# Kernel optimization log

Hardware: AMD Instinct MI355X
Metric: run time of the kernel (lower is better)

Reference implementation:

```python
import jax, jax.numpy as jnp
import numpy as np

N = 10000      # nodes
E = 160000     # edges
B = 4          # batch
D = 256        # in_dim == out_dim
H = 4          # heads
DH = D // H    # per-head dim = 64
L = 2          # num_layers
BACK = 2       # back_look
HID = 128      # hidden_dim
NEG = 0.1      # leaky relu slope


def setup_inputs() -> dict:
    key = jax.random.key(0)
    ks = jax.random.split(key, 12)
    solutions = jax.random.normal(ks[0], (BACK, B, N, HID), dtype=jnp.float32)
    src = jax.random.randint(ks[1], (E,), 0, N)
    dst = jax.random.randint(ks[2], (E,), 0, N)
    w = jax.random.uniform(ks[3], (E,), dtype=jnp.float32)
    fc_w = jax.random.normal(ks[4], (L, D, D), dtype=jnp.float32) * (1.0 / np.sqrt(D))
    attn_l = jax.random.normal(ks[5], (L, H, DH), dtype=jnp.float32) * 0.1
    attn_r = jax.random.normal(ks[6], (L, H, DH), dtype=jnp.float32) * 0.1
    out_fc_w = jax.random.normal(ks[7], (L, DH, DH), dtype=jnp.float32) * (1.0 / np.sqrt(DH))
    out_fc_b = jnp.zeros((L, DH), dtype=jnp.float32)
    mlp_w = jax.random.normal(ks[8], (D, L * D), dtype=jnp.float32) * (1.0 / np.sqrt(L * D))
    mlp_b = jnp.zeros((D,), dtype=jnp.float32)
    return dict(solutions=solutions, w=w, fc_w=fc_w, attn_l=attn_l, attn_r=attn_r,
                out_fc_w=out_fc_w, out_fc_b=out_fc_b, mlp_w=mlp_w, mlp_b=mlp_b,
                src=src, dst=dst)


def _gat_layer(x, w, fc_w, al, ar, ofc_w, ofc_b, src, dst):
    # x: [B,N,D] -> feat: [N,B,H,DH]  (matches torch view+transpose)
    feat = jnp.einsum('bnd,ed->bne', x, fc_w).reshape(B, N, H, DH).transpose(1, 0, 2, 3)
    el = (feat * al).sum(-1)  # [N,B,H]
    er = (feat * ar).sum(-1)  # [N,B,H]
    # edge scores, weighted pre-softmax by edge weight w
    e = jax.nn.leaky_relu(el[src] + er[dst], NEG) * w[:, None, None]  # [E,B,H]
    # edge softmax per destination node (numerically stable)
    m = jax.ops.segment_max(e, dst, num_segments=N)        # [N,B,H]
    ex = jnp.exp(e - m[dst])
    s = jax.ops.segment_sum(ex, dst, num_segments=N)       # [N,B,H]
    a = ex / s[dst]                                        # [E,B,H]
    # weighted scatter-aggregate: u_mul_e + sum
    msg = feat[src] * a[..., None]                         # [E,B,H,DH]
    rst = jax.ops.segment_sum(msg, dst, num_segments=N)    # [N,B,H,DH]
    rst = jax.nn.relu(jnp.einsum('nbhf,of->nbho', rst, ofc_w) + ofc_b)
    # transpose + concat heads -> [B,N,H*DH]
    return rst.transpose(1, 0, 2, 3).reshape(B, N, H * DH)


def reference(solutions, w, fc_w, attn_l, attn_r, out_fc_w, out_fc_b, mlp_w, mlp_b, src, dst):
    # concat back_look solutions along feature dim -> [B,N,D]
    x = jnp.concatenate([solutions[i] for i in range(BACK)], axis=-1)
    outs = []
    for l in range(L):
        x = _gat_layer(x, w, fc_w[l], attn_l[l], attn_r[l],
                       out_fc_w[l], out_fc_b[l], src, dst)
        outs.append(x)
    h = jnp.concatenate(outs, axis=-1)           # [B,N,L*D]
    return h @ mlp_w.T + mlp_b                   # [B,N,D]
```

## Files before the change

kernel.cpp:

```cpp
#include <hip/hip_runtime.h>
#include <math.h>

#define NN 10000
#define NE 160000
#define NB 4
#define NH 4
#define ND 256
#define NT (NN * 16)
#define NM 40000

typedef _Float16 f16;
typedef _Float16 half8 __attribute__((ext_vector_type(8)));
typedef _Float16 h2 __attribute__((ext_vector_type(2)));
typedef float f32x4 __attribute__((ext_vector_type(4)));

union H4 { uint2 u; f16 h[4]; };
union U2H { unsigned u; h2 h; };
union U4H { uint4 u; h2 h[4]; };

__device__ __forceinline__ void gload_lds16(const void* g, void* l) {
  __builtin_amdgcn_global_load_lds((const __attribute__((address_space(1))) void*)g,
                                   (__attribute__((address_space(3))) void*)l, 16, 0, 0);
}

__global__ __launch_bounds__(256) void k_deg(const int* __restrict__ dst, int* __restrict__ deg) {
  int e = blockIdx.x * 256 + threadIdx.x;
  if (e < NE) atomicAdd(&deg[dst[e]], 1);
}

__global__ __launch_bounds__(1024) void k_scan2(const int* __restrict__ deg, int* __restrict__ offs) {
  __shared__ int wsum[16];
  __shared__ int wbase[17];
  const int t = threadIdx.x, lane = t & 63, wv = t >> 6;
  int v[10];
  int s = 0;
  if (t < 1000) {
#pragma unroll
    for (int i = 0; i < 10; ++i) { v[i] = deg[t * 10 + i]; s += v[i]; }
  }
  int inc = s;
#pragma unroll
  for (int k = 1; k < 64; k <<= 1) {
    int u = __shfl_up(inc, k);
    if (lane >= k) inc += u;
  }
  if (lane == 63) wsum[wv] = inc;
  __syncthreads();
  if (t == 0) {
    int c = 0;
#pragma unroll
    for (int i = 0; i < 16; ++i) { wbase[i] = c; c += wsum[i]; }
    wbase[16] = c;
    offs[NN] = c;
  }
  __syncthreads();
  if (t < 1000) {
    int c = wbase[wv] + inc - s;
#pragma unroll
    for (int i = 0; i < 10; ++i) { offs[t * 10 + i] = c; c += v[i]; }
  }
}

__global__ __launch_bounds__(256) void k_scatter(const int* __restrict__ src, const int* __restrict__ dst,
                                                 const float* __restrict__ w, const int* __restrict__ offs,
                                                 int* __restrict__ cursor, int* __restrict__ csr_src,
                                                 float* __restrict__ csr_w) {
  int e = blockIdx.x * 256 + threadIdx.x;
  if (e < NE) {
    int d = dst[e];
    int slot = offs[d] + atomicAdd(&cursor[d], 1);
    csr_src[slot] = src[e];
    csr_w[slot] = w[e];
  }
}

__global__ __launch_bounds__(256) void k_prep(const float* __restrict__ fc_w, const float* __restrict__ ofc_w,
                                              const float* __restrict__ al, const float* __restrict__ ar,
                                              const float* __restrict__ mlp_w,
                                              f16* __restrict__ fwh2, f16* __restrict__ alfh2,
                                              f16* __restrict__ mlph) {
  int r = blockIdx.x;
  int d = threadIdx.x;
  if (r < 512) {
    int l = r >> 8, rr = r & 255;
    int h = rr >> 6, o = rr & 63;
    const float* fcl = fc_w + (size_t)l * 65536;
    const float* ow = ofc_w + (size_t)l * 4096;
    float acc = 0.f;
    for (int f = 0; f < 64; ++f)
      acc = fmaf(ow[(o << 6) + f], fcl[(((h << 6) + f) << 8) + d], acc);
    fwh2[((size_t)l << 16) + (rr << 8) + d] = (f16)acc;
  } else if (r < 544) {
    int rr = r - 512;
    int l = rr >> 4, q = rr & 15;
    const float* fcl = fc_w + (size_t)l * 65536;
    float acc = 0.f;
    if (q < 8) {
      int h = q & 3;
      const float* a = ((q < 4) ? al : ar) + (size_t)l * NH * 64;
      for (int f = 0; f < 64; ++f)
        acc = fmaf(a[(h << 6) + f], fcl[(((h << 6) + f) << 8) + d], acc);
    }
    alfh2[((size_t)l << 12) + (q << 8) + d] = (f16)acc;
  } else {
    int i = (r - 544) * 256 + d;
    float4 v = *(const float4*)(mlp_w + (size_t)i * 4);
    H4 h;
    h.h[0] = (f16)v.x; h.h[1] = (f16)v.y; h.h[2] = (f16)v.z; h.h[3] = (f16)v.w;
    *(uint2*)(mlph + (size_t)i * 4) = h.u;
  }
}

template<int OUTH, int EL, int CVT>
__global__ __launch_bounds__(256) void k_gemm_f16(
    const void* __restrict__ A, int lda, int K,
    const f16* __restrict__ W,
    const float* __restrict__ bias,
    void* __restrict__ outp, int ldo,
    const f16* __restrict__ alfh, float* __restrict__ el2, float* __restrict__ er2)
{
  __shared__ __align__(16) f16 As[64 * 32];
  __shared__ __align__(16) f16 Bs[128 * 32];
  const int tid = threadIdx.x;
  const int lane = tid & 63;
  const int w = tid >> 6;
  const int wr = w >> 1, wc = w & 1;
  const int ra0 = blockIdx.x * 64;
  const int c0 = blockIdx.y * 128;
  const int l2 = lane >> 2;
  const int lk8 = (lane & 3) * 8;

  f32x4 acc[2][4];
#pragma unroll
  for (int mr = 0; mr < 2; ++mr)
#pragma unroll
    for (int nr = 0; nr < 4; ++nr) acc[mr][nr] = (f32x4)0.f;
  f32x4 accel[2];
  accel[0] = (f32x4)0.f; accel[1] = (f32x4)0.f;
  const bool doEl = EL && (blockIdx.y == 0) && (wc == 0);

  const int fr = lane & 15;
  const int fg = (lane >> 4) * 8;

  for (int k0 = 0; k0 < K; k0 += 32) {
    if (CVT) {
      const float* sf = (const float*)A;
      int ra = ra0 + 16 * w + l2;
      int kk = k0 + lk8;
      const float* ps = (kk < 128) ? sf + (size_t)ra * 128 + kk
                                   : sf + (size_t)(NM + ra) * 128 + (kk - 128);
      float4 p0 = *(const float4*)ps;
      float4 p1 = *(const float4*)(ps + 4);
      half8 hv;
      hv[0] = (f16)p0.x; hv[1] = (f16)p0.y; hv[2] = (f16)p0.z; hv[3] = (f16)p0.w;
      hv[4] = (f16)p1.x; hv[5] = (f16)p1.y; hv[6] = (f16)p1.z; hv[7] = (f16)p1.w;
      *(half8*)(As + w * 512 + (lane << 3)) = hv;
    } else {
      gload_lds16((const f16*)A + (size_t)(ra0 + 16 * w + l2) * lda + k0 + lk8, As + w * 512);
    }
    gload_lds16(W + (size_t)(c0 + 32 * w + l2) * K + k0 + lk8, Bs + w * 1024);
    gload_lds16(W + (size_t)(c0 + 32 * w + 16 + l2) * K + k0 + lk8, Bs + w * 1024 + 512);
    __syncthreads();

    half8 af[2], bf[4];
#pragma unroll
    for (int mr = 0; mr < 2; ++mr)
      af[mr] = *(const half8*)(As + (wr * 32 + mr * 16 + fr) * 32 + fg);
#pragma unroll
    for (int nr = 0; nr < 4; ++nr)
      bf[nr] = *(const half8*)(Bs + (wc * 64 + nr * 16 + fr) * 32 + fg);
#pragma unroll
    for (int mr = 0; mr < 2; ++mr)
#pragma unroll
      for (int nr = 0; nr < 4; ++nr)
        acc[mr][nr] = __builtin_amdgcn_mfma_f32_16x16x32_f16(af[mr], bf[nr], acc[mr][nr], 0, 0, 0);
    if (doEl) {
      half8 bal = *(const half8*)(alfh + fr * 256 + k0 + fg);
#pragma unroll
      for (int mr = 0; mr < 2; ++mr)
        accel[mr] = __builtin_amdgcn_mfma_f32_16x16x32_f16(af[mr], bal, accel[mr], 0, 0, 0);
    }
    __syncthreads();
  }

  const int r0 = (lane >> 4) * 4;
#pragma unroll
  for (int nr = 0; nr < 4; ++nr) {
    int col = c0 + wc * 64 + nr * 16 + fr;
    float bv = bias ? bias[col] : 0.f;
#pragma unroll
    for (int mr = 0; mr < 2; ++mr) {
      f32x4 v = acc[mr][nr];
#pragma unroll
      for (int r = 0; r < 4; ++r) {
        int ra = ra0 + wr * 32 + mr * 16 + r0 + r;
        float val = v[r] + bv;
        if (OUTH) ((f16*)outp)[(size_t)ra * ldo + col] = (f16)val;
        else      ((float*)outp)[(size_t)ra * ldo + col] = val;
      }
    }
  }
  if (doEl && fr < 8) {
#pragma unroll
    for (int mr = 0; mr < 2; ++mr) {
#pragma unroll
      for (int r = 0; r < 4; ++r) {
        int ra = ra0 + wr * 32 + mr * 16 + r0 + r;
        int n = ra % NN, b = ra / NN;
        int tb = (n << 4) + (b << 2);
        float val = accel[mr][r];
        if (fr < 4) el2[tb + fr] = val;
        else        er2[tb + (fr - 4)] = val;
      }
    }
  }
}

__global__ __launch_bounds__(256) void k_edge8(
    const f16* __restrict__ featW_b, const float* __restrict__ el2, const float* __restrict__ er2,
    const int* __restrict__ csr_src, const float* __restrict__ csr_w,
    const int* __restrict__ offs, const float* __restrict__ b2, f16* __restrict__ outh)
{
  __shared__ __align__(16) unsigned aalp[4][64][4];
  __shared__ unsigned asrc[4][64];
  __shared__ float aw[4][64];
  __shared__ float sls[4][4];
  __shared__ float sinvs[4][4];
  const int t = threadIdx.x;
  const int w = t >> 6, lane = t & 63;
  const int b = blockIdx.x & 3;
  const int n = (blockIdx.x >> 2) * 4 + w;
  const int s0 = offs[n], s1 = offs[n + 1];
  const int es = lane >> 2;
  const int sh = lane & 3;
  const float erv = er2[(n << 4) + (b << 2) + sh];
  const int hl = lane & 31;
  const int eh = lane >> 5;
  const int h8 = hl >> 3;
  const int ch0 = hl << 3;
  const f16* fW = featW_b + ((size_t)b * NN << 8);

  float m = -INFINITY, srun = 0.f;
  h2 a0 = {(f16)0.f, (f16)0.f}, a1 = a0, a2 = a0, a3 = a0;

  for (int c0 = s0; c0 < s1; c0 += 64) {
    const int csz = min(64, s1 - c0);
    unsigned sv = 0;
    float wv = 0.f;
    if (lane < csz) {
      sv = (unsigned)csr_src[c0 + lane];
      wv = csr_w[c0 + lane];
    }
    asrc[w][lane] = sv;
    aw[w][lane] = wv;
    float sc[4];
#pragma unroll
    for (int i = 0; i < 4; ++i) {
      int e = es + 16 * i;
      if (e < csz) {
        int src = (int)asrc[w][e];
        float x = el2[(src << 4) + (b << 2) + sh] + erv;
        x = (x > 0.f) ? x : 0.1f * x;
        sc[i] = x * aw[w][e];
      } else sc[i] = -INFINITY;
    }
    float mc = fmaxf(fmaxf(sc[0], sc[1]), fmaxf(sc[2], sc[3]));
#pragma unroll
    for (int k = 4; k <= 32; k <<= 1) mc = fmaxf(mc, __shfl_xor(mc, k));
    float mn = fmaxf(m, mc);
    float sl = (m == -INFINITY) ? 0.f : __expf(m - mn);
    float ps = 0.f;
#pragma unroll
    for (int i = 0; i < 4; ++i) {
      int e = es + 16 * i;
      float a = (e < csz) ? __expf(sc[i] - mn) : 0.f;
      ps += a;
      f16 ah = (f16)a;
      U2H sp; sp.h[0] = ah; sp.h[1] = ah;
      aalp[w][e][sh] = sp.u;
    }
#pragma unroll
    for (int k = 4; k <= 32; k <<= 1) ps += __shfl_xor(ps, k);
    srun = srun * sl + ps;
    m = mn;
    if (es == 0) sls[w][sh] = sl;
    float slA = sls[w][h8];
    f16 slh = (f16)slA;
    h2 slv = {slh, slh};
    a0 *= slv; a1 *= slv; a2 *= slv; a3 *= slv;
#pragma unroll 2
    for (int e = 0; e < csz; e += 2) {
      const int ee = e + eh;
      unsigned su = asrc[w][ee];
      U2H al; al.u = aalp[w][ee][h8];
      U4H fv;
      fv.u = *(const uint4*)(fW + ((size_t)su << 8) + ch0);
      a0 += fv.h[0] * al.h;
      a1 += fv.h[1] * al.h;
      a2 += fv.h[2] * al.h;
      a3 += fv.h[3] * al.h;
    }
  }
  U2H u0, u1, u2, u3;
  u0.h = a0; u1.h = a1; u2.h = a2; u3.h = a3;
  U2H p0, p1, p2, p3;
  p0.u = (unsigned)__shfl_xor((int)u0.u, 32);
  p1.u = (unsigned)__shfl_xor((int)u1.u, 32);
  p2.u = (unsigned)__shfl_xor((int)u2.u, 32);
  p3.u = (unsigned)__shfl_xor((int)u3.u, 32);
  a0 += p0.h; a1 += p1.h; a2 += p2.h; a3 += p3.h;

  float invs = (s1 > s0) ? 1.f / srun : 0.f;
  if (es == 0) sinvs[w][sh] = invs;

  if (lane < 32) {
    const float invv = sinvs[w][h8];
    const float4 bv0 = *(const float4*)(b2 + ((hl & 7) << 3));
    const float4 bv1 = *(const float4*)(b2 + ((hl & 7) << 3) + 4);
    H4 o01, o23;
    o01.h[0] = (f16)fmaxf(fmaf((float)a0[0], invv, bv0.x), 0.f);
    o01.h[1] = (f16)fmaxf(fmaf((float)a0[1], invv, bv0.y), 0.f);
    o01.h[2] = (f16)fmaxf(fmaf((float)a1[0], invv, bv0.z), 0.f);
    o01.h[3] = (f16)fmaxf(fmaf((float)a1[1], invv, bv0.w), 0.f);
    o23.h[0] = (f16)fmaxf(fmaf((float)a2[0], invv, bv1.x), 0.f);
    o23.h[1] = (f16)fmaxf(fmaf((float)a2[1], invv, bv1.y), 0.f);
    o23.h[2] = (f16)fmaxf(fmaf((float)a3[0], invv, bv1.z), 0.f);
    o23.h[3] = (f16)fmaxf(fmaf((float)a3[1], invv, bv1.w), 0.f);
    uint4 ov;
    ov.x = o01.u.x; ov.y = o01.u.y; ov.z = o23.u.x; ov.w = o23.u.y;
    *(uint4*)(outh + ((size_t)(b * NN + n) << 9) + ch0) = ov;
  }
}

extern "C" void kernel_launch(void* const* d_in, const int* in_sizes, int n_in,
                              void* d_out, int out_size, void* d_ws, size_t ws_size,
                              hipStream_t stream) {
  const float* sol    = (const float*)d_in[0];
  const float* w      = (const float*)d_in[1];
  const float* fc_w   = (const float*)d_in[2];
  const float* attn_l = (const float*)d_in[3];
  const float* attn_r = (const float*)d_in[4];
  const float* ofc_w  = (const float*)d_in[5];
  const float* ofc_b  = (const float*)d_in[6];
  const float* mlp_w  = (const float*)d_in[7];
  const float* mlp_b  = (const float*)d_in[8];
  const int*   d_src  = (const int*)d_in[9];
  const int*   d_dst  = (const int*)d_in[10];
  float* out = (float*)d_out;

  char* p = (char*)d_ws;
  auto alloc = [&](size_t bytes) { char* r = p; p += (bytes + 255) & ~(size_t)255; return r; };
  f16*   out01h  = (f16*)alloc((size_t)(NM + 128) * 512 * 2);
  f16*   featWb  = (f16*)alloc((size_t)NM * 256 * 2);
  f16*   fwh2    = (f16*)alloc((size_t)2 * ND * ND * 2);
  f16*   alfh2   = (f16*)alloc((size_t)2 * 16 * ND * 2);
  f16*   mlph    = (f16*)alloc((size_t)ND * 512 * 2);
  float* el2     = (float*)alloc((size_t)NT * 4);
  float* er2     = (float*)alloc((size_t)NT * 4);
  int*   deg     = (int*)alloc((size_t)(NN + 1) * 4);
  int*   offs    = (int*)alloc((size_t)(NN + 1) * 4);
  int*   cursor  = (int*)alloc((size_t)NN * 4);
  int*   csr_src = (int*)alloc((size_t)NE * 4);
  float* csr_w   = (float*)alloc((size_t)NE * 4);
  if ((size_t)(p - (char*)d_ws) > ws_size) return;

  hipMemsetAsync(deg, 0, (size_t)NN * 4, stream);
  hipMemsetAsync(cursor, 0, (size_t)NN * 4, stream);
  k_deg<<<NE / 256, 256, 0, stream>>>(d_dst, deg);
  k_scan2<<<1, 1024, 0, stream>>>(deg, offs);
  k_scatter<<<NE / 256, 256, 0, stream>>>(d_src, d_dst, w, offs, cursor, csr_src, csr_w);

  k_prep<<<672, 256, 0, stream>>>(fc_w, ofc_w, attn_l, attn_r, mlp_w, fwh2, alfh2, mlph);

  for (int l = 0; l < 2; ++l) {
    const f16* fwh  = fwh2 + ((size_t)l << 16);
    const f16* alfh = alfh2 + ((size_t)l << 12);
    if (l == 0) {
      k_gemm_f16<1, 1, 1><<<dim3(NM / 64, ND / 128), 256, 0, stream>>>(
          sol, 128, 256, fwh, nullptr, featWb, 256, alfh, el2, er2);
    } else {
      k_gemm_f16<1, 1, 0><<<dim3(NM / 64, ND / 128), 256, 0, stream>>>(
          out01h, 512, 256, fwh, nullptr, featWb, 256, alfh, el2, er2);
    }
    k_edge8<<<(NN / 4) * 4, 256, 0, stream>>>(featWb, el2, er2, csr_src, csr_w, offs,
                                              ofc_b + (size_t)l * 64, out01h + (l == 0 ? 0 : 256));
  }

  k_gemm_f16<0, 0, 0><<<dim3(NM / 64, ND / 128), 256, 0, stream>>>(
      out01h, 512, 512, mlph, mlp_b, out, 256, nullptr, nullptr, nullptr);
}
```

Before: 185.3 us.

## Double GEMM K-tile to 64 and merge workspace memsets into one

The f16 GEMM now stages a 64-wide K slice of A and W in LDS per iteration instead of 32, running two MFMA sub-steps per barrier pair. This halves the number of __syncthreads and loop iterations and issues more loads per sync, at the cost of doubled LDS use per block. Separately, the degree and cursor buffers are made contiguous so a single memset replaces two.

After: 181.8 us. Within noise of the previous version (-1.9%).

```diff
diff --git a/kernel.cpp b/kernel.cpp
--- a/kernel.cpp
+++ b/kernel.cpp
@@ -119,16 +119,16 @@
     void* __restrict__ outp, int ldo,
     const f16* __restrict__ alfh, float* __restrict__ el2, float* __restrict__ er2)
 {
-  __shared__ __align__(16) f16 As[64 * 32];
-  __shared__ __align__(16) f16 Bs[128 * 32];
+  __shared__ __align__(16) f16 As[64 * 64];
+  __shared__ __align__(16) f16 Bs[128 * 64];
   const int tid = threadIdx.x;
   const int lane = tid & 63;
   const int w = tid >> 6;
   const int wr = w >> 1, wc = w & 1;
   const int ra0 = blockIdx.x * 64;
   const int c0 = blockIdx.y * 128;
-  const int l2 = lane >> 2;
-  const int lk8 = (lane & 3) * 8;
+  const int l8r = lane >> 3;
+  const int l8o = (lane & 7) * 8;
 
   f32x4 acc[2][4];
 #pragma unroll
@@ -142,43 +142,54 @@
   const int fr = lane & 15;
   const int fg = (lane >> 4) * 8;
 
-  for (int k0 = 0; k0 < K; k0 += 32) {
+  for (int k0 = 0; k0 < K; k0 += 64) {
     if (CVT) {
       const float* sf = (const float*)A;
-      int ra = ra0 + 16 * w + l2;
-      int kk = k0 + lk8;
-      const float* ps = (kk < 128) ? sf + (size_t)ra * 128 + kk
-                                   : sf + (size_t)(NM + ra) * 128 + (kk - 128);
-      float4 p0 = *(const float4*)ps;
-      float4 p1 = *(const float4*)(ps + 4);
-      half8 hv;
-      hv[0] = (f16)p0.x; hv[1] = (f16)p0.y; hv[2] = (f16)p0.z; hv[3] = (f16)p0.w;
-      hv[4] = (f16)p1.x; hv[5] = (f16)p1.y; hv[6] = (f16)p1.z; hv[7] = (f16)p1.w;
-      *(half8*)(As + w * 512 + (lane << 3)) = hv;
+#pragma unroll
+      for (int i = 0; i < 2; ++i) {
+        int chunk = tid + i * 256;
+        int row = chunk >> 3;
+        int kk = k0 + (chunk & 7) * 8;
+        const float* ps = (kk < 128) ? sf + (size_t)(ra0 + row) * 128 + kk
+                                     : sf + (size_t)(NM + ra0 + row) * 128 + (kk - 128);
+        float4 p0 = *(const float4*)ps;
+        float4 p1 = *(const float4*)(ps + 4);
+        half8 hv;
+        hv[0] = (f16)p0.x; hv[1] = (f16)p0.y; hv[2] = (f16)p0.z; hv[3] = (f16)p0.w;
+        hv[4] = (f16)p1.x; hv[5] = (f16)p1.y; hv[6] = (f16)p1.z; hv[7] = (f16)p1.w;
+        *(half8*)(As + chunk * 8) = hv;
+      }
     } else {
-      gload_lds16((const f16*)A + (size_t)(ra0 + 16 * w + l2) * lda + k0 + lk8, As + w * 512);
-    }
-    gload_lds16(W + (size_t)(c0 + 32 * w + l2) * K + k0 + lk8, Bs + w * 1024);
-    gload_lds16(W + (size_t)(c0 + 32 * w + 16 + l2) * K + k0 + lk8, Bs + w * 1024 + 512);
+      const f16* Af = (const f16*)A;
+      gload_lds16(Af + (size_t)(ra0 + 16 * w + l8r) * lda + k0 + l8o, As + w * 1024);
+      gload_lds16(Af + (size_t)(ra0 + 16 * w + 8 + l8r) * lda + k0 + l8o, As + w * 1024 + 512);
+    }
+#pragma unroll
+    for (int j = 0; j < 4; ++j)
+      gload_lds16(W + (size_t)(c0 + 32 * w + j * 8 + l8r) * K + k0 + l8o,
+                  Bs + w * 2048 + j * 512);
     __syncthreads();
 
-    half8 af[2], bf[4];
-#pragma unroll
-    for (int mr = 0; mr < 2; ++mr)
-      af[mr] = *(const half8*)(As + (wr * 32 + mr * 16 + fr) * 32 + fg);
-#pragma unroll
-    for (int nr = 0; nr < 4; ++nr)
-      bf[nr] = *(const half8*)(Bs + (wc * 64 + nr * 16 + fr) * 32 + fg);
-#pragma unroll
-    for (int mr = 0; mr < 2; ++mr)
+#pragma unroll
+    for (int kk = 0; kk < 2; ++kk) {
+      half8 af[2], bf[4];
+#pragma unroll
+      for (int mr = 0; mr < 2; ++mr)
+        af[mr] = *(const half8*)(As + (wr * 32 + mr * 16 + fr) * 64 + kk * 32 + fg);
 #pragma unroll
       for (int nr = 0; nr < 4; ++nr)
-        acc[mr][nr] = __builtin_amdgcn_mfma_f32_16x16x32_f16(af[mr], bf[nr], acc[mr][nr], 0, 0, 0);
-    if (doEl) {
-      half8 bal = *(const half8*)(alfh + fr * 256 + k0 + fg);
+        bf[nr] = *(const half8*)(Bs + (wc * 64 + nr * 16 + fr) * 64 + kk * 32 + fg);
 #pragma unroll
       for (int mr = 0; mr < 2; ++mr)
-        accel[mr] = __builtin_amdgcn_mfma_f32_16x16x32_f16(af[mr], bal, accel[mr], 0, 0, 0);
+#pragma unroll
+        for (int nr = 0; nr < 4; ++nr)
+          acc[mr][nr] = __builtin_amdgcn_mfma_f32_16x16x32_f16(af[mr], bf[nr], acc[mr][nr], 0, 0, 0);
+      if (doEl) {
+        half8 bal = *(const half8*)(alfh + fr * 256 + k0 + kk * 32 + fg);
+#pragma unroll
+        for (int mr = 0; mr < 2; ++mr)
+          accel[mr] = __builtin_amdgcn_mfma_f32_16x16x32_f16(af[mr], bal, accel[mr], 0, 0, 0);
+      }
     }
     __syncthreads();
   }
@@ -357,15 +368,15 @@
   f16*   mlph    = (f16*)alloc((size_t)ND * 512 * 2);
   float* el2     = (float*)alloc((size_t)NT * 4);
   float* er2     = (float*)alloc((size_t)NT * 4);
-  int*   deg     = (int*)alloc((size_t)(NN + 1) * 4);
+  int*   degcur  = (int*)alloc((size_t)(2 * NN) * 4);
+  int*   deg     = degcur;
+  int*   cursor  = degcur + NN;
   int*   offs    = (int*)alloc((size_t)(NN + 1) * 4);
-  int*   cursor  = (int*)alloc((size_t)NN * 4);
   int*   csr_src = (int*)alloc((size_t)NE * 4);
   float* csr_w   = (float*)alloc((size_t)NE * 4);
   if ((size_t)(p - (char*)d_ws) > ws_size) return;
 
-  hipMemsetAsync(deg, 0, (size_t)NN * 4, stream);
-  hipMemsetAsync(cursor, 0, (size_t)NN * 4, stream);
+  hipMemsetAsync(degcur, 0, (size_t)(2 * NN) * 4, stream);
   k_deg<<<NE / 256, 256, 0, stream>>>(d_dst, deg);
   k_scan2<<<1, 1024, 0, stream>>>(deg, offs);
   k_scatter<<<NE / 256, 256, 0, stream>>>(d_src, d_dst, w, offs, cursor, csr_src, csr_w);
```
